# Optimization experiments

Hardware: AMD Instinct MI355X
Metric: run time of the kernel (lower is better)

Reference implementation:

```python
import jax, jax.numpy as jnp
import numpy as np

NUM_OBJ_CLS = 151  # Visual Genome object classes


def setup_inputs() -> dict:
    key = jax.random.key(0)
    ks = jax.random.split(key, 10)
    N_OBJ, HIDDEN, POOL, N_REL, N_RELCLS = 8192, 512, 4096, 32768, 51
    s = lambda d: 1.0 / np.sqrt(d)
    return {
        "edge_ctx": jax.random.normal(ks[0], (N_OBJ, HIDDEN), jnp.float32),
        "rel_pair_idx": jax.random.randint(ks[1], (N_REL, 2), 0, N_OBJ, jnp.int64),
        "union_features": jax.random.normal(ks[2], (N_REL, POOL), jnp.float32),
        "W_obj": jax.random.normal(ks[3], (HIDDEN, NUM_OBJ_CLS), jnp.float32) * s(HIDDEN),
        "b_obj": jnp.zeros((NUM_OBJ_CLS,), jnp.float32),
        "W_post_emb": jax.random.normal(ks[4], (HIDDEN, 2 * HIDDEN), jnp.float32) * s(HIDDEN),
        "b_post_emb": jnp.zeros((2 * HIDDEN,), jnp.float32),
        "W_post_cat": jax.random.normal(ks[5], (2 * HIDDEN, POOL), jnp.float32) * s(2 * HIDDEN),
        "b_post_cat": jnp.zeros((POOL,), jnp.float32),
        "W_rel": jax.random.normal(ks[6], (POOL, N_RELCLS), jnp.float32) * s(POOL),
        "b_rel": jnp.zeros((N_RELCLS,), jnp.float32),
        "freq_bias": jax.random.normal(ks[7], (NUM_OBJ_CLS * NUM_OBJ_CLS, N_RELCLS), jnp.float32),
    }


def reference(edge_ctx, rel_pair_idx, union_features, W_obj, b_obj,
              W_post_emb, b_post_emb, W_post_cat, b_post_cat, W_rel, b_rel,
              freq_bias):
    hidden = edge_ctx.shape[-1]
    # object classifier (stand-in for context layer's obj head)
    obj_dists = edge_ctx @ W_obj + b_obj                       # [N_obj, 151]
    obj_preds = jnp.argmax(obj_dists, axis=-1)                 # [N_obj]
    # post_emb -> split into head / tail representations
    edge_rep = (edge_ctx @ W_post_emb + b_post_emb).reshape(-1, 2, hidden)
    head_rep = edge_rep[:, 0]                                  # [N_obj, hidden]
    tail_rep = edge_rep[:, 1]
    # gather pair reps (global indices == per-image split + local gather + cat)
    h_idx, t_idx = rel_pair_idx[:, 0], rel_pair_idx[:, 1]
    prod_rep = jnp.concatenate([head_rep[h_idx], tail_rep[t_idx]], axis=-1)  # [N_rel, 2*hidden]
    prod_rep = prod_rep @ W_post_cat + b_post_cat              # [N_rel, pool]
    prod_rep = prod_rep * union_features                       # use_vision
    rel_dists = prod_rep @ W_rel + b_rel                       # [N_rel, 51]
    # frequency bias lookup on predicted (head, tail) label pairs
    pair_lbl = obj_preds[h_idx] * NUM_OBJ_CLS + obj_preds[t_idx]
    rel_dists = rel_dists + freq_bias[pair_lbl]
    return rel_dists
```

## Files before the change

kernel.cpp:

```cpp
#include <hip/hip_runtime.h>
#include <hip/hip_bf16.h>
#include <hip/hip_fp16.h>

typedef _Float16 f16;
typedef _Float16 f16x8 __attribute__((ext_vector_type(8)));
typedef _Float16 f16x4 __attribute__((ext_vector_type(4)));
typedef float f32x4 __attribute__((ext_vector_type(4)));

#define N_OBJ 8192
#define HIDDEN 512
#define POOL 4096
#define N_REL 32768
#define N_RELCLS 51
#define NUM_OBJ_CLS 151

#define WS_E16    0UL
#define WS_WPE16  8388608UL
#define WS_WCATT  9437184UL
#define WS_FT     17825792UL
#define WS_P      26214400UL
#define WS_BIAS   160432128UL
#define WS_PREDS  160448512UL
#define WS_WFRAG  160481280UL

typedef const __attribute__((address_space(1))) void* gas_ptr;
typedef __attribute__((address_space(3))) void* las_ptr;
__device__ __forceinline__ void gl_lds16(const f16* g, f16* l) {
    __builtin_amdgcn_global_load_lds((gas_ptr)g, (las_ptr)l, 16, 0, 0);
}

#define OPB 8
__global__ __launch_bounds__(256) void k_prep(const float* __restrict__ edge_ctx, const float* __restrict__ Wpe,
                                              const float* __restrict__ Wcat, const float* __restrict__ bpe,
                                              const float* __restrict__ bcat, const float* __restrict__ Wrel,
                                              const float* __restrict__ Wobj, const float* __restrict__ bobj,
                                              f16* __restrict__ E16, f16* __restrict__ Wpe16,
                                              f16* __restrict__ WcatT, float* __restrict__ bias,
                                              f16* __restrict__ wfrag, int* __restrict__ preds) {
    __shared__ float se[OPB * HIDDEN];
    __shared__ double part[2][OPB][5][32];
    __shared__ double redv[OPB][32];
    __shared__ int    redj[OPB][32];
    __shared__ float tile[32][33];
    __shared__ float red[8][32];
    int bid = blockIdx.x, tid = threadIdx.x;
    if (bid < 1024) {
        int o0 = bid * OPB;
        const f32x4* Ev = (const f32x4*)(edge_ctx + (size_t)o0 * HIDDEN);
        f32x4* sev = (f32x4*)se;
        #pragma unroll
        for (int i = 0; i < OPB * HIDDEN / 4 / 256; i++)
            sev[tid + i * 256] = Ev[tid + i * 256];
        __syncthreads();
        int ks = tid >> 5;
        int jg = tid & 31;
        int jgc = (jg < 31) ? jg : 30;
        double acc[OPB][5];
        #pragma unroll
        for (int o = 0; o < OPB; o++)
            #pragma unroll
            for (int jj = 0; jj < 5; jj++) acc[o][jj] = 0.0;
        int kbase = ks * 64;
        for (int k4 = 0; k4 < 16; k4++) {
            int k = kbase + k4 * 4;
            f32x4 ev[OPB];
            #pragma unroll
            for (int o = 0; o < OPB; o++) ev[o] = *(const f32x4*)(se + o * HIDDEN + k);
            #pragma unroll
            for (int kk = 0; kk < 4; kk++) {
                const float* wrow = Wobj + (size_t)(k + kk) * NUM_OBJ_CLS;
                float wv[5];
                #pragma unroll
                for (int jj = 0; jj < 5; jj++) {
                    int j = jj * 31 + jgc;
                    wv[jj] = wrow[(j < NUM_OBJ_CLS) ? j : (NUM_OBJ_CLS - 1)];
                }
                #pragma unroll
                for (int o = 0; o < OPB; o++) {
                    double e = (double)ev[o][kk];
                    #pragma unroll
                    for (int jj = 0; jj < 5; jj++)
                        acc[o][jj] = fma(e, (double)wv[jj], acc[o][jj]);
                }
            }
        }
        #pragma unroll
        for (int o = 0; o < OPB; o++)
            #pragma unroll
            for (int jj = 0; jj < 5; jj++)
                acc[o][jj] += __shfl_xor(acc[o][jj], 32);
        int w = tid >> 6, lane = tid & 63;
        if (w >= 2 && lane < 32) {
            #pragma unroll
            for (int o = 0; o < OPB; o++)
                #pragma unroll
                for (int jj = 0; jj < 5; jj++) part[w - 2][o][jj][lane] = acc[o][jj];
        }
        __syncthreads();
        if (w < 2 && lane < 32) {
            #pragma unroll
            for (int o = 0; o < OPB; o++)
                #pragma unroll
                for (int jj = 0; jj < 5; jj++) acc[o][jj] += part[w][o][jj][lane];
        }
        __syncthreads();
        if (w == 1 && lane < 32) {
            #pragma unroll
            for (int o = 0; o < OPB; o++)
                #pragma unroll
                for (int jj = 0; jj < 5; jj++) part[0][o][jj][lane] = acc[o][jj];
        }
        __syncthreads();
        if (w == 0 && lane < 31) {
            #pragma unroll
            for (int o = 0; o < OPB; o++) {
                double best = -1e300; int bj = NUM_OBJ_CLS;
                #pragma unroll
                for (int jj = 0; jj < 5; jj++) {
                    int j = jj * 31 + lane;
                    if (j < NUM_OBJ_CLS) {
                        double v = acc[o][jj] + part[0][o][jj][lane] + (double)bobj[j];
                        if (v > best || (v == best && j < bj)) { best = v; bj = j; }
                    }
                }
                redv[o][lane] = best; redj[o][lane] = bj;
            }
        }
        __syncthreads();
        if (tid < OPB) {
            int o = tid;
            double best = -1e300; int bj = NUM_OBJ_CLS;
            for (int g = 0; g < 31; g++) {
                double v = redv[o][g]; int j = redj[o][g];
                if (v > best || (v == best && j < bj)) { best = v; bj = j; }
            }
            preds[o0 + o] = bj;
        }
    } else if (bid < 2048) {
        const f32x4* in = (const f32x4*)edge_ctx;
        f16x4* out = (f16x4*)E16;
        int base = (bid - 1024) * 1024 + tid;
        #pragma unroll
        for (int s = 0; s < 4; s++) {
            f32x4 v = in[base + s * 256];
            f16x4 h; h[0]=(f16)v[0]; h[1]=(f16)v[1]; h[2]=(f16)v[2]; h[3]=(f16)v[3];
            out[base + s * 256] = h;
        }
    } else if (bid < 2176) {
        const f32x4* in = (const f32x4*)Wpe;
        f16x4* out = (f16x4*)Wpe16;
        int base = (bid - 2048) * 1024 + tid;
        #pragma unroll
        for (int s = 0; s < 4; s++) {
            f32x4 v = in[base + s * 256];
            f16x4 h; h[0]=(f16)v[0]; h[1]=(f16)v[1]; h[2]=(f16)v[2]; h[3]=(f16)v[3];
            out[base + s * 256] = h;
        }
    } else if (bid < 6272) {
        int t = bid - 2176;
        int c0 = (t & 127) * 32, r0 = (t >> 7) * 32;
        int tx = tid & 31, ty = tid >> 5;
        #pragma unroll
        for (int i = 0; i < 4; i++)
            tile[ty + 8 * i][tx] = Wcat[(size_t)(r0 + ty + 8 * i) * POOL + c0 + tx];
        __syncthreads();
        #pragma unroll
        for (int i = 0; i < 4; i++)
            WcatT[(size_t)(c0 + ty + 8 * i) * (2 * HIDDEN) + r0 + tx] = (f16)tile[tx][ty + 8 * i];
    } else if (bid < 6400) {
        int c = (bid - 6272) * 32 + (tid & 31);
        int jq = tid >> 5;
        float acc = 0.0f;
        #pragma unroll 4
        for (int j = jq * 128; j < jq * 128 + 128; j++)
            acc += bpe[j] * Wcat[(size_t)j * POOL + c];
        red[jq][tid & 31] = acc;
        __syncthreads();
        if (jq == 0) {
            float s = bcat[c];
            #pragma unroll
            for (int q = 0; q < 8; q++) s += red[q][tid & 31];
            bias[c] = s;
        }
    } else {
        int kstep = bid - 6400;
        int lane = tid & 63;
        int nt = tid >> 6;
        int n = nt * 16 + (lane & 15);
        int k0 = kstep * 32 + (lane >> 4) * 8;
        f16x8 v;
        #pragma unroll
        for (int jj = 0; jj < 8; jj++) {
            float w = (n < N_RELCLS) ? Wrel[(size_t)(k0 + jj) * N_RELCLS + n] : 0.0f;
            v[jj] = (f16)w;
        }
        ((f16x8*)wfrag)[(size_t)(kstep * 4 + nt) * 64 + lane] = v;
    }
}

template<bool SPLITM>
__global__ __launch_bounds__(256) void k_gemm(const f16* __restrict__ A, const f16* __restrict__ B,
                                              f16* __restrict__ C, const float* __restrict__ bias,
                                              int K, int lda, int ldb, int ldc,
                                              long aZ, long bZ, long cZ, int biasLimit) {
    __shared__ f16 As[2][128 * 32];
    __shared__ f16 Bs[2][128 * 32];
    long z = blockIdx.z;
    A += z * aZ; B += z * bZ; C += z * cZ;

    int tid = threadIdx.x;
    int w = tid >> 6, lane = tid & 63;
    int wm = w >> 1, wn = w & 1;
    int lr = lane & 15, lg = lane >> 4;
    int mBase = blockIdx.y * 128;
    int nBase = blockIdx.x * 128;

    const f16* aSrc[2]; const f16* bSrc[2];
    f16* aDst[2]; f16* bDst[2];
    #pragma unroll
    for (int p = 0; p < 2; p++) {
        int c = p * 256 + tid;
        int row = c >> 2, slot = c & 3;
        int g = (slot ^ ((row ^ (row >> 2)) & 3)) * 8;
        aSrc[p] = A + (size_t)(mBase + row) * lda + g;
        bSrc[p] = B + (size_t)(nBase + row) * ldb + g;
        aDst[p] = As[0] + p * 2048 + w * 512;
        bDst[p] = Bs[0] + p * 2048 + w * 512;
    }
    int swzL = ((lr & 3) ^ ((lr >> 2) & 3)) * 8;
    f32x4 acc[4][4] = {};
    int nt = K >> 5;

    #pragma unroll
    for (int p = 0; p < 2; p++) { gl_lds16(aSrc[p], aDst[p]); gl_lds16(bSrc[p], bDst[p]); }

    for (int t = 0; t < nt; t++) {
        __syncthreads();
        int cur = t & 1;
        if (t + 1 < nt) {
            int koff = (t + 1) * 32;
            int nxt = (cur ^ 1) * 4096;
            #pragma unroll
            for (int p = 0; p < 2; p++) {
                gl_lds16(aSrc[p] + koff, aDst[p] + nxt);
                gl_lds16(bSrc[p] + koff, bDst[p] + nxt);
            }
        }
        const f16* Ab = As[cur];
        const f16* Bb = Bs[cur];
        f16x8 av[4], bv[4];
        #pragma unroll
        for (int i = 0; i < 4; i++) {
            av[i] = *(const f16x8*)(Ab + (wm * 64 + i * 16 + lr) * 32 + ((lg * 8) ^ swzL));
            bv[i] = *(const f16x8*)(Bb + (wn * 64 + i * 16 + lr) * 32 + ((lg * 8) ^ swzL));
        }
        #pragma unroll
        for (int i = 0; i < 4; i++)
            #pragma unroll
            for (int jj = 0; jj < 4; jj++)
                acc[i][jj] = __builtin_amdgcn_mfma_f32_16x16x32_f16(av[i], bv[jj], acc[i][jj], 0, 0, 0);
    }

    #pragma unroll
    for (int i = 0; i < 4; i++) {
        int mb = mBase + wm * 64 + i * 16 + lg * 4;
        f32x4 bi = {};
        if (bias && mb < biasLimit) bi = *(const f32x4*)(bias + mb);
        #pragma unroll
        for (int jj = 0; jj < 4; jj++) {
            int n = nBase + wn * 64 + jj * 16 + lr;
            f16x4 hv;
            #pragma unroll
            for (int r = 0; r < 4; r++) hv[r] = (f16)(acc[i][jj][r] + bi[r]);
            if (SPLITM) {
                size_t off = ((size_t)((mb >= POOL) ? N_OBJ : 0) + n) * POOL + (mb & (POOL - 1));
                *(f16x4*)(C + off) = hv;
            } else {
                *(f16x4*)(C + (size_t)n * ldc + mb) = hv;
            }
        }
    }
}

__global__ __launch_bounds__(256) void k_final(const f16* __restrict__ P, const float* __restrict__ U,
                                               const int* __restrict__ relp, const int* __restrict__ preds,
                                               const f16* __restrict__ wfrag, const float* __restrict__ brel,
                                               const float* __restrict__ fbias, float* __restrict__ out) {
    int w = threadIdx.x >> 6;
    int lane = threadIdx.x & 63;
    int lr = lane & 15, lg = lane >> 4;
    int r0 = blockIdx.x * 64 + w * 16;
    int arow = r0 + lr;
    int h = relp[2 * arow], t = relp[2 * arow + 1];
    const f16* ph = P + (size_t)h * POOL;
    const f16* pt = P + (size_t)(N_OBJ + t) * POOL;
    const float* u = U + (size_t)arow * POOL;
    f32x4 acc[4] = {};
    for (int ks = 0; ks < POOL / 32; ks++) {
        int ka = ks * 32 + lg * 8;
        f16x8 vh = *(const f16x8*)(ph + ka);
        f16x8 vt = *(const f16x8*)(pt + ka);
        f32x4 u0 = __builtin_nontemporal_load((const f32x4*)(u + ka));
        f32x4 u1 = __builtin_nontemporal_load((const f32x4*)(u + ka + 4));
        f16x8 a;
        #pragma unroll
        for (int jj = 0; jj < 8; jj++) {
            float uu = (jj < 4) ? u0[jj] : u1[jj - 4];
            a[jj] = (f16)(((float)vh[jj] + (float)vt[jj]) * uu);
        }
        const f16x8* bf = (const f16x8*)wfrag + (size_t)ks * 4 * 64 + lane;
        #pragma unroll
        for (int nt = 0; nt < 4; nt++)
            acc[nt] = __builtin_amdgcn_mfma_f32_16x16x32_f16(a, bf[nt * 64], acc[nt], 0, 0, 0);
    }
    #pragma unroll
    for (int r = 0; r < 4; r++) {
        int row = r0 + lg * 4 + r;
        int h2 = relp[2 * row], t2 = relp[2 * row + 1];
        int lbl = preds[h2] * NUM_OBJ_CLS + preds[t2];
        const float* fb = fbias + (size_t)lbl * N_RELCLS;
        #pragma unroll
        for (int nt = 0; nt < 4; nt++) {
            int j = nt * 16 + lr;
            if (j < N_RELCLS)
                out[(size_t)row * N_RELCLS + j] = acc[nt][r] + brel[j] + fb[j];
        }
    }
}

extern "C" void kernel_launch(void* const* d_in, const int* in_sizes, int n_in,
                              void* d_out, int out_size, void* d_ws, size_t ws_size,
                              hipStream_t stream) {
    const float* edge_ctx = (const float*)d_in[0];
    const int*   relp     = (const int*)d_in[1];
    const float* U        = (const float*)d_in[2];
    const float* Wobj     = (const float*)d_in[3];
    const float* bobj     = (const float*)d_in[4];
    const float* Wpe      = (const float*)d_in[5];
    const float* bpe      = (const float*)d_in[6];
    const float* Wcat     = (const float*)d_in[7];
    const float* bcat     = (const float*)d_in[8];
    const float* Wrel     = (const float*)d_in[9];
    const float* brel     = (const float*)d_in[10];
    const float* fbias    = (const float*)d_in[11];
    float* out = (float*)d_out;

    char* ws = (char*)d_ws;
    f16*   E16    = (f16*)(ws + WS_E16);
    f16*   Wpe16  = (f16*)(ws + WS_WPE16);
    f16*   WcatT  = (f16*)(ws + WS_WCATT);
    f16*   FT     = (f16*)(ws + WS_FT);
    f16*   P      = (f16*)(ws + WS_P);
    float* bias   = (float*)(ws + WS_BIAS);
    int*   preds  = (int*)(ws + WS_PREDS);
    f16*   wfrag  = (f16*)(ws + WS_WFRAG);

    k_prep<<<6528, 256, 0, stream>>>(edge_ctx, Wpe, Wcat, bpe, bcat, Wrel, Wobj, bobj,
                                     E16, Wpe16, WcatT, bias, wfrag, preds);
    k_gemm<false><<<dim3(POOL / 128, HIDDEN / 128, 2), 256, 0, stream>>>(
        Wpe16, WcatT, FT, nullptr, HIDDEN, 2 * HIDDEN, 2 * HIDDEN, HIDDEN,
        512L, 512L, (long)POOL * HIDDEN, 0);
    k_gemm<true><<<dim3(N_OBJ / 128, (2 * POOL) / 128, 1), 256, 0, stream>>>(
        FT, E16, P, bias, HIDDEN, HIDDEN, HIDDEN, POOL,
        0L, 0L, 0L, POOL);
    k_final<<<N_REL / 64, 256, 0, stream>>>(P, U, relp, preds, wfrag, brel, fbias, out);
}
```

Baseline: 390.7 us.

## Bucket relations by head object and swizzle final blocks for locality

Builds a counting-sort permutation of relations keyed on head object index (groups of 8). It adds a histogram pass in the prep kernel, a scan kernel and a scatter kernel. The final kernel processes rows in this permuted order, with a block-index swizzle spread across XCDs, so that gathered head rows of P are reused from cache. This adds three small launches plus atomics. The union_features reads become non-sequential per block, since they are now gathered per row.

```diff
diff --git a/kernel.cpp b/kernel.cpp
--- a/kernel.cpp
+++ b/kernel.cpp
@@ -22,6 +22,10 @@
 #define WS_BIAS   160432128UL
 #define WS_PREDS  160448512UL
 #define WS_WFRAG  160481280UL
+#define WS_PERM   161005568UL
+#define WS_HIST   161136640UL
+#define WS_BASE   161140736UL
+#define WS_CURS   161144832UL
 
 typedef const __attribute__((address_space(1))) void* gas_ptr;
 typedef __attribute__((address_space(3))) void* las_ptr;
@@ -34,9 +38,11 @@
                                               const float* __restrict__ Wcat, const float* __restrict__ bpe,
                                               const float* __restrict__ bcat, const float* __restrict__ Wrel,
                                               const float* __restrict__ Wobj, const float* __restrict__ bobj,
+                                              const int* __restrict__ relp,
                                               f16* __restrict__ E16, f16* __restrict__ Wpe16,
                                               f16* __restrict__ WcatT, float* __restrict__ bias,
-                                              f16* __restrict__ wfrag, int* __restrict__ preds) {
+                                              f16* __restrict__ wfrag, int* __restrict__ preds,
+                                              int* __restrict__ hist) {
     __shared__ float se[OPB * HIDDEN];
     __shared__ double part[2][OPB][5][32];
     __shared__ double redv[OPB][32];
@@ -182,7 +188,7 @@
             for (int q = 0; q < 8; q++) s += red[q][tid & 31];
             bias[c] = s;
         }
-    } else {
+    } else if (bid < 6528) {
         int kstep = bid - 6400;
         int lane = tid & 63;
         int nt = tid >> 6;
@@ -195,7 +201,35 @@
             v[jj] = (f16)w;
         }
         ((f16x8*)wfrag)[(size_t)(kstep * 4 + nt) * 64 + lane] = v;
-    }
+    } else {
+        int r = (bid - 6528) * 256 + tid;
+        atomicAdd(&hist[relp[2 * r] >> 3], 1);
+    }
+}
+
+__global__ __launch_bounds__(1024) void k_scan(const int* __restrict__ hist, int* __restrict__ base,
+                                               int* __restrict__ cursor) {
+    __shared__ int s[1024];
+    int t = threadIdx.x;
+    int v = hist[t];
+    s[t] = v;
+    __syncthreads();
+    for (int off = 1; off < 1024; off <<= 1) {
+        int x = (t >= off) ? s[t - off] : 0;
+        __syncthreads();
+        s[t] += x;
+        __syncthreads();
+    }
+    base[t] = s[t] - v;
+    cursor[t] = 0;
+}
+
+__global__ __launch_bounds__(256) void k_scatter(const int* __restrict__ relp, const int* __restrict__ base,
+                                                 int* __restrict__ cursor, int* __restrict__ perm) {
+    int r = blockIdx.x * 256 + threadIdx.x;
+    int b = relp[2 * r] >> 3;
+    int slot = base[b] + atomicAdd(&cursor[b], 1);
+    perm[slot] = r;
 }
 
 template<bool SPLITM>
@@ -285,12 +319,18 @@
 __global__ __launch_bounds__(256) void k_final(const f16* __restrict__ P, const float* __restrict__ U,
                                                const int* __restrict__ relp, const int* __restrict__ preds,
                                                const f16* __restrict__ wfrag, const float* __restrict__ brel,
-                                               const float* __restrict__ fbias, float* __restrict__ out) {
+                                               const float* __restrict__ fbias, const int* __restrict__ perm,
+                                               float* __restrict__ out) {
+    int nb = gridDim.x;
+    int chunk = nb >> 3;
+    int bid = blockIdx.x;
+    int sw = (bid & 7) * chunk + (bid >> 3);
+
     int w = threadIdx.x >> 6;
     int lane = threadIdx.x & 63;
     int lr = lane & 15, lg = lane >> 4;
-    int r0 = blockIdx.x * 64 + w * 16;
-    int arow = r0 + lr;
+    int r0 = sw * 64 + w * 16;
+    int arow = perm[r0 + lr];
     int h = relp[2 * arow], t = relp[2 * arow + 1];
     const f16* ph = P + (size_t)h * POOL;
     const f16* pt = P + (size_t)(N_OBJ + t) * POOL;
@@ -315,7 +355,7 @@
     }
     #pragma unroll
     for (int r = 0; r < 4; r++) {
-        int row = r0 + lg * 4 + r;
+        int row = perm[r0 + lg * 4 + r];
         int h2 = relp[2 * row], t2 = relp[2 * row + 1];
         int lbl = preds[h2] * NUM_OBJ_CLS + preds[t2];
         const float* fb = fbias + (size_t)lbl * N_RELCLS;
@@ -354,14 +394,21 @@
     float* bias   = (float*)(ws + WS_BIAS);
     int*   preds  = (int*)(ws + WS_PREDS);
     f16*   wfrag  = (f16*)(ws + WS_WFRAG);
-
-    k_prep<<<6528, 256, 0, stream>>>(edge_ctx, Wpe, Wcat, bpe, bcat, Wrel, Wobj, bobj,
-                                     E16, Wpe16, WcatT, bias, wfrag, preds);
+    int*   perm   = (int*)(ws + WS_PERM);
+    int*   hist   = (int*)(ws + WS_HIST);
+    int*   basep  = (int*)(ws + WS_BASE);
+    int*   curs   = (int*)(ws + WS_CURS);
+
+    hipMemsetAsync(hist, 0, 1024 * sizeof(int), stream);
+    k_prep<<<6656, 256, 0, stream>>>(edge_ctx, Wpe, Wcat, bpe, bcat, Wrel, Wobj, bobj, relp,
+                                     E16, Wpe16, WcatT, bias, wfrag, preds, hist);
+    k_scan<<<1, 1024, 0, stream>>>(hist, basep, curs);
+    k_scatter<<<N_REL / 256, 256, 0, stream>>>(relp, basep, curs, perm);
     k_gemm<false><<<dim3(POOL / 128, HIDDEN / 128, 2), 256, 0, stream>>>(
         Wpe16, WcatT, FT, nullptr, HIDDEN, 2 * HIDDEN, 2 * HIDDEN, HIDDEN,
         512L, 512L, (long)POOL * HIDDEN, 0);
     k_gemm<true><<<dim3(N_OBJ / 128, (2 * POOL) / 128, 1), 256, 0, stream>>>(
         FT, E16, P, bias, HIDDEN, HIDDEN, HIDDEN, POOL,
         0L, 0L, 0L, POOL);
-    k_final<<<N_REL / 64, 256, 0, stream>>>(P, U, relp, preds, wfrag, brel, fbias, out);
-}
+    k_final<<<N_REL / 64, 256, 0, stream>>>(P, U, relp, preds, wfrag, brel, fbias, perm, out);
+}
```

Result: slower. 422.9 us (+8.2%).
